# Kernel tuning notes

Measured on AMD Instinct MI355X. Metric: run time of the kernel, lower is better.

## Reference

```python
import jax, jax.numpy as jnp
import numpy as np
import math

B, T, C, E, H = 16, 256, 6, 512, 8


def setup_inputs() -> dict:
    key = jax.random.key(0)
    ks = jax.random.split(key, 5)
    std = 0.02
    return {
        "x": jax.random.normal(ks[0], (B, T, C, E), dtype=jnp.float32),
        "Wq": jax.random.normal(ks[1], (E, E), dtype=jnp.float32) * std,
        "bq": jnp.zeros((E,), dtype=jnp.float32),
        "Wk": jax.random.normal(ks[2], (E, E), dtype=jnp.float32) * std,
        "bk": jnp.zeros((E,), dtype=jnp.float32),
        "Wv": jax.random.normal(ks[3], (E, E), dtype=jnp.float32) * std,
        "bv": jnp.zeros((E,), dtype=jnp.float32),
        "Wp": jax.random.normal(ks[4], (E, E), dtype=jnp.float32) * std,
        "bp": jnp.zeros((E,), dtype=jnp.float32),
    }


def reference(x, Wq, bq, Wk, bk, Wv, bv, Wp, bp):
    b, t, c, e = x.shape
    hd = e // H
    # nn.Linear: y = x @ W^T + b, then view(B,T,C,H,hd).transpose(1,3) -> (B,H,C,T,hd)
    def heads(W, bias):
        y = jnp.einsum('btce,fe->btcf', x, W) + bias
        return y.reshape(b, t, c, H, hd).transpose(0, 3, 2, 1, 4)  # B,H,C,T,hd

    q = heads(Wq, bq)
    k = heads(Wk, bk)
    v = heads(Wv, bv)

    scale = 1.0 / math.sqrt(hd)
    att = jnp.einsum('bhctd,bhcsd->bhcts', q, k) * scale  # B,H,C,T,T
    causal = jnp.tril(jnp.ones((t, t), dtype=bool))
    att = jnp.where(causal, att, -jnp.inf)
    att = jax.nn.softmax(att, axis=-1)

    y = jnp.einsum('bhcts,bhcsd->bhctd', att, v)  # B,H,C,T,hd
    # permute(0,3,1,2,4) -> (B,T,H,C,hd), then view(B,T,C,E) (faithful to torch)
    y = y.transpose(0, 3, 1, 2, 4).reshape(b, t, c, e)
    return jnp.einsum('btce,fe->btcf', y, Wp) + bp
```

## Files before the change

### kernel.cpp

```cpp
#include <hip/hip_runtime.h>


typedef unsigned short u16;
typedef short bf16x8 __attribute__((ext_vector_type(8)));
typedef float f32x4 __attribute__((ext_vector_type(4)));
typedef u16 u16x4 __attribute__((ext_vector_type(4)));

#define MFMA16(a, b, c) __builtin_amdgcn_mfma_f32_16x16x32_bf16((a), (b), (c), 0, 0, 0)

__device__ __forceinline__ u16 f2b(float f) {
  union { float f; unsigned u; } v; v.f = f;
  unsigned r = v.u + 0x7fffu + ((v.u >> 16) & 1u);
  return (u16)(r >> 16);
}
__device__ __forceinline__ void gl_lds16(const void* g, void* l) {
  __builtin_amdgcn_global_load_lds(
      (const __attribute__((address_space(1))) void*)g,
      (__attribute__((address_space(3))) void*)l, 16, 0, 0);
}

__global__ void cvt_all(const float* __restrict__ x, u16* __restrict__ xdst,
                        const float* W0, const float* W1, const float* W2,
                        const float* W3, u16* __restrict__ wdst, int nxb) {
  const int bx = blockIdx.x;
  if (bx < nxb) {
    const size_t idx = ((size_t)bx * 256 + threadIdx.x) * 4;
    f32x4 v = *(const f32x4*)(x + idx);
    u16x4 o; o.x = f2b(v.x); o.y = f2b(v.y); o.z = f2b(v.z); o.w = f2b(v.w);
    *(u16x4*)(xdst + idx) = o;
  } else {
    const int wb = bx - nxb;
    const float* src = (wb < 256) ? W0 : (wb < 512) ? W1
                     : (wb < 768) ? W2 : W3;
    const int idx = ((wb & 255) * 256 + threadIdx.x) * 4;
    f32x4 v = *(const f32x4*)(src + idx);
    u16x4 o; o.x = f2b(v.x); o.y = f2b(v.y); o.z = f2b(v.z); o.w = f2b(v.w);
    *(u16x4*)(wdst + (size_t)(wb >> 8) * 262144 + idx) = o;
  }
}

#define STAGE(k, bi) do { \
  char* Sd_ = Sb + (bi) * 28672; \
  _Pragma("unroll") \
  for (int j_ = 0; j_ < 4; ++j_) \
    if (j_ < 3 || tid < 256) \
      gl_lds16(gsrc[j_] + (k) * 64, Sd_ + fl[j_]); \
} while (0)

__global__ __launch_bounds__(512, 2) void qkv_attn(
    const u16* __restrict__ xbf, const u16* __restrict__ wbf,
    const float* __restrict__ bq, const float* __restrict__ bk,
    const float* __restrict__ bv, u16* __restrict__ y_ws)
{
  const int blk = blockIdx.x;
  const int b   = blk / 48;
  const int h   = (blk / 6) % 8;
  const int c   = blk % 6;

  __shared__ u16 LDS[43008];
  char* Ksb  = (char*)LDS;
  char* Vtsb = (char*)LDS + 16384;
  char* Sb   = (char*)LDS;

  const int tid  = threadIdx.x;
  const int lane = tid & 63;
  const int wv   = tid >> 6;
  const int r    = lane & 15;
  const int qd   = lane >> 4;
  const int tiles[2] = { wv, 15 - wv };
  char* Qw = (char*)LDS + 32768 + wv * 2048;

  const char* gsrc[4]; int fl[4];
  #pragma unroll
  for (int j = 0; j < 4; ++j) {
    const int idx  = j * 512 + tid;
    const int flat = idx * 16;
    const int row  = flat >> 6;
    const int gc   = (((flat >> 4) & 3) - (row >> 1)) & 3;
    fl[j] = flat;
    if (row < 256) {
      gsrc[j] = (const char*)xbf +
                ((size_t)(b * 256 + row) * 6 + c) * 1024 + gc * 16;
    } else {
      const int wr  = row - 256;
      const int tau = (wr >> 6) & 3;
      const int n   = wr & 63;
      gsrc[j] = (const char*)wbf + (size_t)tau * 524288 +
                (size_t)(h * 64 + n) * 1024 + gc * 16;
    }
  }

  int aoff[2], boff[3][4];
  #pragma unroll
  for (int ti = 0; ti < 2; ++ti) {
    const int row = tiles[ti] * 16 + r;
    aoff[ti] = row * 64 + ((qd + (row >> 1)) & 3) * 16;
  }
  #pragma unroll
  for (int tau = 0; tau < 3; ++tau)
    #pragma unroll
    for (int nt = 0; nt < 4; ++nt) {
      const int row = 256 + tau * 64 + nt * 16 + r;
      boff[tau][nt] = row * 64 + ((qd + (row >> 1)) & 3) * 16;
    }

  f32x4 acc[3][2][4] = {};

  STAGE(0, 0);
  STAGE(1, 1);

  #pragma unroll 2
  for (int kt = 0; kt < 16; ++kt) {
    if (kt < 15) { asm volatile("s_waitcnt vmcnt(3)\n\ts_barrier" ::: "memory"); }
    else         { asm volatile("s_waitcnt vmcnt(0)\n\ts_barrier" ::: "memory"); }

    if (kt + 2 < 16) STAGE(kt + 2, (kt + 2) % 3);

    char* Sc = Sb + (kt % 3) * 28672;
    bf16x8 af[2], bfr[3][4];
    #pragma unroll
    for (int ti = 0; ti < 2; ++ti)
      af[ti] = *(const bf16x8*)(Sc + aoff[ti]);
    #pragma unroll
    for (int tau = 0; tau < 3; ++tau)
      #pragma unroll
      for (int nt = 0; nt < 4; ++nt)
        bfr[tau][nt] = *(const bf16x8*)(Sc + boff[tau][nt]);

    #pragma unroll
    for (int tau = 0; tau < 3; ++tau)
      #pragma unroll
      for (int ti = 0; ti < 2; ++ti)
        #pragma unroll
        for (int nt = 0; nt < 4; ++nt)
          acc[tau][ti][nt] = MFMA16(af[ti], bfr[tau][nt], acc[tau][ti][nt]);
  }
  __syncthreads();

  float bqv[4], bkv[4], bvv[4];
  #pragma unroll
  for (int nt = 0; nt < 4; ++nt) {
    const int col = h * 64 + nt * 16 + r;
    bqv[nt] = bq[col]; bkv[nt] = bk[col]; bvv[nt] = bv[col];
  }

  const int lo0 = ( qd      ^ (r & 7)) << 4;
  const int lo1 = ((4 + qd) ^ (r & 7)) << 4;

  f32x4 o_acc[2][4] = {};
  float l_acc[2][4] = {{0.f,0.f,0.f,0.f},{0.f,0.f,0.f,0.f}};

  #pragma unroll
  for (int sc = 0; sc < 2; ++sc) {
    if (sc) __syncthreads();

    {
      const int tl0 = tiles[sc] * 16 + qd * 4 - sc * 128;
      #pragma unroll
      for (int nt = 0; nt < 4; ++nt) {
        u16x4 pv;
        #pragma unroll
        for (int rr = 0; rr < 4; ++rr)
          ((u16*)&pv)[rr] = f2b(acc[2][sc][nt][rr] + bvv[nt]);
        const int vb = (nt * 16 + r) * 256 +
            (((tl0 >> 3) ^ (r & 7)) << 4) + (tl0 & 7) * 2;
        *(u16x4*)(Vtsb + vb) = pv;
      }
      #pragma unroll
      for (int nt = 0; nt < 4; ++nt)
        #pragma unroll
        for (int rr = 0; rr < 4; ++rr) {
          const int tl = tl0 + rr;
          const int kb = tl * 128 +
              (((nt * 2 + (r >> 3)) ^ (tl & 7)) << 4) + (r & 7) * 2;
          *(u16*)(Ksb + kb) = f2b(acc[1][sc][nt][rr] + bkv[nt]);
        }
    }
    __syncthreads();

    #pragma unroll
    for (int ti = 0; ti < 2; ++ti) {
      if (sc == 1 && ti == 0) continue;
      const int mt  = tiles[ti];
      const int i0  = mt * 16;
      const int nch = (mt >> 2) + 1;

      #pragma unroll
      for (int nt = 0; nt < 4; ++nt)
        #pragma unroll
        for (int rr = 0; rr < 4; ++rr) {
          const int prow = qd * 4 + rr;
          const int qb = prow * 128 +
              (((nt * 2 + (r >> 3)) ^ (prow & 7)) << 4) + (r & 7) * 2;
          *(u16*)(Qw + qb) = f2b(acc[0][ti][nt][rr] + bqv[nt]);
        }
      asm volatile("s_waitcnt lgkmcnt(0)" ::: "memory");

      bf16x8 qf[2];
      qf[0] = *(const bf16x8*)(Qw + r * 128 + lo0);
      qf[1] = *(const bf16x8*)(Qw + r * 128 + lo1);
      asm volatile("s_waitcnt lgkmcnt(0)" ::: "memory");

      #pragma unroll
      for (int jcl = 0; jcl < 2; ++jcl) {
        const int jcg = sc * 2 + jcl;
        if (jcg >= nch) continue;
        const int j0l = jcl * 64;
        const int j0g = jcg * 64;

        f32x4 s[4] = {};
        #pragma unroll
        for (int nt = 0; nt < 4; ++nt) {
          const int krow = j0l + nt * 16 + r;
          bf16x8 kf0 = *(const bf16x8*)(Ksb + krow * 128 + lo0);
          s[nt] = MFMA16(qf[0], kf0, s[nt]);
          bf16x8 kf1 = *(const bf16x8*)(Ksb + krow * 128 + lo1);
          s[nt] = MFMA16(qf[1], kf1, s[nt]);
        }

        #pragma unroll
        for (int nt = 0; nt < 4; ++nt)
          #pragma unroll
          for (int rr = 0; rr < 4; ++rr) {
            const int i = i0 + qd * 4 + rr;
            const int j = j0g + nt * 16 + r;
            float p = __builtin_exp2f(fminf(s[nt][rr], 500.f) *
                                      0.1803368801111244f);
            if (j > i) p = 0.f;
            l_acc[ti][rr] += p;
            const int prow = qd * 4 + rr;
            const int pb = prow * 128 +
                (((nt * 2 + (r >> 3)) ^ (prow & 7)) << 4) + (r & 7) * 2;
            *(u16*)(Qw + pb) = f2b(p);
          }
        asm volatile("s_waitcnt lgkmcnt(0)" ::: "memory");

        bf16x8 pf[2];
        pf[0] = *(const bf16x8*)(Qw + r * 128 + lo0);
        pf[1] = *(const bf16x8*)(Qw + r * 128 + lo1);
        #pragma unroll
        for (int ntd = 0; ntd < 4; ++ntd) {
          const int vrow = ntd * 16 + r;
          bf16x8 vf0 = *(const bf16x8*)(Vtsb + vrow * 256 +
              ((((j0l >> 3) + qd) ^ (r & 7)) << 4));
          o_acc[ti][ntd] = MFMA16(pf[0], vf0, o_acc[ti][ntd]);
          bf16x8 vf1 = *(const bf16x8*)(Vtsb + vrow * 256 +
              ((((j0l >> 3) + 4 + qd) ^ (r & 7)) << 4));
          o_acc[ti][ntd] = MFMA16(pf[1], vf1, o_acc[ti][ntd]);
        }
      }
    }
  }

  const size_t obase = ((size_t)b * 256) * 3072 + h * 384 + c * 64;
  #pragma unroll
  for (int ti = 0; ti < 2; ++ti) {
    const int i0 = tiles[ti] * 16;
    float linv[4];
    #pragma unroll
    for (int rr = 0; rr < 4; ++rr) {
      float sum = l_acc[ti][rr];
      sum += __shfl_xor(sum, 1, 16);
      sum += __shfl_xor(sum, 2, 16);
      sum += __shfl_xor(sum, 4, 16);
      sum += __shfl_xor(sum, 8, 16);
      linv[rr] = 1.f / sum;
    }
    #pragma unroll
    for (int ntd = 0; ntd < 4; ++ntd)
      #pragma unroll
      for (int rr = 0; rr < 4; ++rr) {
        const int t = i0 + qd * 4 + rr;
        const int d = ntd * 16 + r;
        y_ws[obase + (size_t)t * 3072 + d] = f2b(o_acc[ti][ntd][rr] * linv[rr]);
      }
  }
}

__global__ __launch_bounds__(256, 3) void gemm_bt(
    const u16* __restrict__ A,
    const u16* W0, const u16* W1, const u16* W2,
    const float* bs0, const float* bs1, const float* bs2,
    u16* O0, u16* O1, u16* O2,
    float* OF,
    int qkv_mode)
{
  const int z = blockIdx.z;
  const u16* W    = (z == 0) ? W0 : (z == 1) ? W1 : W2;
  const float* bs = (z == 0) ? bs0 : (z == 1) ? bs1 : bs2;
  u16* O          = (z == 0) ? O0 : (z == 1) ? O1 : O2;

  const int m0 = blockIdx.x * 128;
  const int n0 = blockIdx.y * 128;

  __shared__ u16 As[128 * 32];
  __shared__ u16 Bs[128 * 32];

  const int tid  = threadIdx.x;
  const int lane = tid & 63;
  const int wv   = tid >> 6;
  const int r    = lane & 15;
  const int qd   = lane >> 4;
  const int wm   = (wv & 1) * 64;
  const int wn   = (wv >> 1) * 64;

  f32x4 acc[4][4] = {};

  for (int k0 = 0; k0 < 512; k0 += 32) {
    __syncthreads();
    #pragma unroll
    for (int it = 0; it < 2; ++it) {
      const int flat = (it * 256 + tid) * 16;
      const int row  = flat >> 6;
      const int swc  = (flat >> 4) & 3;
      const int gc   = (swc - (row >> 1)) & 3;
      gl_lds16((const char*)A + (size_t)(m0 + row) * 1024 + k0 * 2 + gc * 16,
               (char*)As + flat);
      gl_lds16((const char*)W + (size_t)(n0 + row) * 1024 + k0 * 2 + gc * 16,
               (char*)Bs + flat);
    }
    __syncthreads();

    bf16x8 af[4], bf[4];
    #pragma unroll
    for (int mt = 0; mt < 4; ++mt) {
      const int row = wm + mt * 16 + r;
      const int sw  = (qd + (row >> 1)) & 3;
      af[mt] = *(const bf16x8*)((const char*)As + row * 64 + sw * 16);
    }
    #pragma unroll
    for (int nt = 0; nt < 4; ++nt) {
      const int row = wn + nt * 16 + r;
      const int sw  = (qd + (row >> 1)) & 3;
      bf[nt] = *(const bf16x8*)((const char*)Bs + row * 64 + sw * 16);
    }
    #pragma unroll
    for (int mt = 0; mt < 4; ++mt)
      #pragma unroll
      for (int nt = 0; nt < 4; ++nt)
        acc[mt][nt] = MFMA16(af[mt], bf[nt], acc[mt][nt]);
  }

  float bv[4];
  #pragma unroll
  for (int nt = 0; nt < 4; ++nt) bv[nt] = bs[n0 + wn + nt * 16 + r];

  if (qkv_mode) {
    #pragma unroll
    for (int mt = 0; mt < 4; ++mt) {
      #pragma unroll
      for (int rr = 0; rr < 4; ++rr) {
        const int m   = m0 + wm + mt * 16 + qd * 4 + rr;
        const int b   = m / 1536;
        const int rem = m - b * 1536;
        const int t   = rem / 6;
        const int c   = rem - t * 6;
        #pragma unroll
        for (int nt = 0; nt < 4; ++nt) {
          const int f = n0 + wn + nt * 16 + r;
          const int hh = f >> 6;
          const int d = f & 63;
          const size_t addr = ((((size_t)b * 8 + hh) * 6 + c) * 256 + t) * 64 + d;
          O[addr] = f2b(acc[mt][nt][rr] + bv[nt]);
        }
      }
    }
  } else {
    #pragma unroll
    for (int mt = 0; mt < 4; ++mt) {
      #pragma unroll
      for (int rr = 0; rr < 4; ++rr) {
        const int m = m0 + wm + mt * 16 + qd * 4 + rr;
        #pragma unroll
        for (int nt = 0; nt < 4; ++nt) {
          const int f = n0 + wn + nt * 16 + r;
          OF[(size_t)m * 512 + f] = acc[mt][nt][rr] + bv[nt];
        }
      }
    }
  }
}

extern "C" void kernel_launch(void* const* d_in, const int* in_sizes, int n_in,
                              void* d_out, int out_size, void* d_ws, size_t ws_size,
                              hipStream_t stream) {
  const float* x  = (const float*)d_in[0];
  const float* Wq = (const float*)d_in[1];
  const float* bq = (const float*)d_in[2];
  const float* Wk = (const float*)d_in[3];
  const float* bk = (const float*)d_in[4];
  const float* Wv = (const float*)d_in[5];
  const float* bv = (const float*)d_in[6];
  const float* Wp = (const float*)d_in[7];
  const float* bp = (const float*)d_in[8];
  float* out = (float*)d_out;

  const size_t PER_B = 256 * 6 * 512;
  const size_t WSEG  = 4 * 262144;

  int NB = 16;
  while (NB > 1 && (WSEG + (size_t)2 * NB * PER_B) * 2 > ws_size) NB >>= 1;

  u16* wbf = (u16*)d_ws;
  u16* Wpb = wbf + 3 * 262144;

  const size_t slab = (size_t)NB * PER_B;
  u16* xbf  = wbf + WSEG;
  u16* y_ws = xbf + slab;

  const int nslab = 16 / NB;
  for (int s = 0; s < nslab; ++s) {
    const float* x_s  = x   + (size_t)s * NB * PER_B;
    float*      out_s = out + (size_t)s * NB * PER_B;
    const int nxb = NB * 768;
    const int grid = (s == 0) ? nxb + 1024 : nxb;
    cvt_all<<<dim3(grid), 256, 0, stream>>>(x_s, xbf, Wq, Wk, Wv, Wp, wbf, nxb);
    qkv_attn<<<dim3(NB * 48), 512, 0, stream>>>(xbf, wbf, bq, bk, bv, y_ws);
    gemm_bt<<<dim3(NB * 12, 4, 1), 256, 0, stream>>>(
        y_ws, Wpb, Wpb, Wpb, bp, bp, bp, nullptr, nullptr, nullptr, out_s, 0);
  }
}
```

Before: 202.0 us.

## Retile QKV projection per wave and stage full Q in shared memory

Each wave now computes a contiguous 64-row by 32-column block of the Q, K and V projections instead of two scattered 16-row tiles across all 64 head columns. This cuts the LDS fragment loads per k-step from 14 to 10 for the same 24 MFMAs. The full biased Q tile is written once to shared memory after the GEMM, replacing the per-tile Q write, waitcnt and readback inside attention. The P scratch moves to a separate LDS region. K/V writes are now split by wave group per half of the sequence, which changes the LDS layout and bookkeeping.

```diff
diff --git a/kernel.cpp b/kernel.cpp
--- a/kernel.cpp
+++ b/kernel.cpp
@@ -60,6 +60,7 @@
   __shared__ u16 LDS[43008];
   char* Ksb  = (char*)LDS;
   char* Vtsb = (char*)LDS + 16384;
+  char* Qsb  = (char*)LDS + 32768;
   char* Sb   = (char*)LDS;
 
   const int tid  = threadIdx.x;
@@ -67,8 +68,10 @@
   const int wv   = tid >> 6;
   const int r    = lane & 15;
   const int qd   = lane >> 4;
+  const int g    = wv >> 1;
+  const int ch   = wv & 1;
   const int tiles[2] = { wv, 15 - wv };
-  char* Qw = (char*)LDS + 32768 + wv * 2048;
+  char* Pw = (char*)LDS + 65536 + wv * 2048;
 
   const char* gsrc[4]; int fl[4];
   #pragma unroll
@@ -82,29 +85,31 @@
       gsrc[j] = (const char*)xbf +
                 ((size_t)(b * 256 + row) * 6 + c) * 1024 + gc * 16;
     } else {
-      const int wr  = row - 256;
-      const int tau = (wr >> 6) & 3;
-      const int n   = wr & 63;
+      const int sr  = row - 256;
+      const int chw = sr / 96;
+      const int rem = sr - chw * 96;
+      const int tau = rem >> 5;
+      const int nn  = rem & 31;
       gsrc[j] = (const char*)wbf + (size_t)tau * 524288 +
-                (size_t)(h * 64 + n) * 1024 + gc * 16;
-    }
-  }
-
-  int aoff[2], boff[3][4];
-  #pragma unroll
-  for (int ti = 0; ti < 2; ++ti) {
-    const int row = tiles[ti] * 16 + r;
-    aoff[ti] = row * 64 + ((qd + (row >> 1)) & 3) * 16;
+                (size_t)(h * 64 + chw * 32 + nn) * 1024 + gc * 16;
+    }
+  }
+
+  int aoff[4], boff[3][2];
+  #pragma unroll
+  for (int mt = 0; mt < 4; ++mt) {
+    const int row = g * 64 + mt * 16 + r;
+    aoff[mt] = row * 64 + ((qd + (row >> 1)) & 3) * 16;
   }
   #pragma unroll
   for (int tau = 0; tau < 3; ++tau)
     #pragma unroll
-    for (int nt = 0; nt < 4; ++nt) {
-      const int row = 256 + tau * 64 + nt * 16 + r;
+    for (int nt = 0; nt < 2; ++nt) {
+      const int row = 256 + ch * 96 + tau * 32 + nt * 16 + r;
       boff[tau][nt] = row * 64 + ((qd + (row >> 1)) & 3) * 16;
     }
 
-  f32x4 acc[3][2][4] = {};
+  f32x4 acc[3][4][2] = {};
 
   STAGE(0, 0);
   STAGE(1, 1);
@@ -117,36 +122,48 @@
     if (kt + 2 < 16) STAGE(kt + 2, (kt + 2) % 3);
 
     char* Sc = Sb + (kt % 3) * 28672;
-    bf16x8 af[2], bfr[3][4];
-    #pragma unroll
-    for (int ti = 0; ti < 2; ++ti)
-      af[ti] = *(const bf16x8*)(Sc + aoff[ti]);
+    bf16x8 af[4], bfr[3][2];
+    #pragma unroll
+    for (int mt = 0; mt < 4; ++mt)
+      af[mt] = *(const bf16x8*)(Sc + aoff[mt]);
     #pragma unroll
     for (int tau = 0; tau < 3; ++tau)
       #pragma unroll
-      for (int nt = 0; nt < 4; ++nt)
+      for (int nt = 0; nt < 2; ++nt)
         bfr[tau][nt] = *(const bf16x8*)(Sc + boff[tau][nt]);
 
     #pragma unroll
     for (int tau = 0; tau < 3; ++tau)
       #pragma unroll
-      for (int ti = 0; ti < 2; ++ti)
-        #pragma unroll
-        for (int nt = 0; nt < 4; ++nt)
-          acc[tau][ti][nt] = MFMA16(af[ti], bfr[tau][nt], acc[tau][ti][nt]);
+      for (int mt = 0; mt < 4; ++mt)
+        #pragma unroll
+        for (int nt = 0; nt < 2; ++nt)
+          acc[tau][mt][nt] = MFMA16(af[mt], bfr[tau][nt], acc[tau][mt][nt]);
   }
   __syncthreads();
 
-  float bqv[4], bkv[4], bvv[4];
-  #pragma unroll
-  for (int nt = 0; nt < 4; ++nt) {
-    const int col = h * 64 + nt * 16 + r;
+  float bqv[2], bkv[2], bvv[2];
+  #pragma unroll
+  for (int nt = 0; nt < 2; ++nt) {
+    const int col = h * 64 + ch * 32 + nt * 16 + r;
     bqv[nt] = bq[col]; bkv[nt] = bk[col]; bvv[nt] = bv[col];
   }
 
   const int lo0 = ( qd      ^ (r & 7)) << 4;
   const int lo1 = ((4 + qd) ^ (r & 7)) << 4;
 
+  #pragma unroll
+  for (int mt = 0; mt < 4; ++mt)
+    #pragma unroll
+    for (int nt = 0; nt < 2; ++nt)
+      #pragma unroll
+      for (int rr = 0; rr < 4; ++rr) {
+        const int t   = g * 64 + mt * 16 + qd * 4 + rr;
+        const int col = ch * 32 + nt * 16 + r;
+        const int qb  = t * 128 + (((col >> 3) ^ (t & 7)) << 4) + (r & 7) * 2;
+        *(u16*)(Qsb + qb) = f2b(acc[0][mt][nt][rr] + bqv[nt]);
+      }
+
   f32x4 o_acc[2][4] = {};
   float l_acc[2][4] = {{0.f,0.f,0.f,0.f},{0.f,0.f,0.f,0.f}};
 
@@ -154,27 +171,30 @@
   for (int sc = 0; sc < 2; ++sc) {
     if (sc) __syncthreads();
 
-    {
-      const int tl0 = tiles[sc] * 16 + qd * 4 - sc * 128;
-      #pragma unroll
-      for (int nt = 0; nt < 4; ++nt) {
-        u16x4 pv;
-        #pragma unroll
-        for (int rr = 0; rr < 4; ++rr)
-          ((u16*)&pv)[rr] = f2b(acc[2][sc][nt][rr] + bvv[nt]);
-        const int vb = (nt * 16 + r) * 256 +
-            (((tl0 >> 3) ^ (r & 7)) << 4) + (tl0 & 7) * 2;
-        *(u16x4*)(Vtsb + vb) = pv;
-      }
-      #pragma unroll
-      for (int nt = 0; nt < 4; ++nt)
-        #pragma unroll
-        for (int rr = 0; rr < 4; ++rr) {
-          const int tl = tl0 + rr;
-          const int kb = tl * 128 +
-              (((nt * 2 + (r >> 3)) ^ (tl & 7)) << 4) + (r & 7) * 2;
-          *(u16*)(Ksb + kb) = f2b(acc[1][sc][nt][rr] + bkv[nt]);
+    if ((g >> 1) == sc) {
+      #pragma unroll
+      for (int mt = 0; mt < 4; ++mt) {
+        const int tl0 = g * 64 + mt * 16 + qd * 4 - sc * 128;
+        #pragma unroll
+        for (int nt = 0; nt < 2; ++nt) {
+          u16x4 pv;
+          #pragma unroll
+          for (int rr = 0; rr < 4; ++rr)
+            ((u16*)&pv)[rr] = f2b(acc[2][mt][nt][rr] + bvv[nt]);
+          const int d  = ch * 32 + nt * 16 + r;
+          const int vb = d * 256 + (((tl0 >> 3) ^ (r & 7)) << 4) + (tl0 & 7) * 2;
+          *(u16x4*)(Vtsb + vb) = pv;
         }
+        #pragma unroll
+        for (int nt = 0; nt < 2; ++nt)
+          #pragma unroll
+          for (int rr = 0; rr < 4; ++rr) {
+            const int tl  = tl0 + rr;
+            const int col = ch * 32 + nt * 16 + r;
+            const int kb  = tl * 128 + (((col >> 3) ^ (tl & 7)) << 4) + (r & 7) * 2;
+            *(u16*)(Ksb + kb) = f2b(acc[1][mt][nt][rr] + bkv[nt]);
+          }
+      }
     }
     __syncthreads();
 
@@ -185,21 +205,9 @@
       const int i0  = mt * 16;
       const int nch = (mt >> 2) + 1;
 
-      #pragma unroll
-      for (int nt = 0; nt < 4; ++nt)
-        #pragma unroll
-        for (int rr = 0; rr < 4; ++rr) {
-          const int prow = qd * 4 + rr;
-          const int qb = prow * 128 +
-              (((nt * 2 + (r >> 3)) ^ (prow & 7)) << 4) + (r & 7) * 2;
-          *(u16*)(Qw + qb) = f2b(acc[0][ti][nt][rr] + bqv[nt]);
-        }
-      asm volatile("s_waitcnt lgkmcnt(0)" ::: "memory");
-
       bf16x8 qf[2];
-      qf[0] = *(const bf16x8*)(Qw + r * 128 + lo0);
-      qf[1] = *(const bf16x8*)(Qw + r * 128 + lo1);
-      asm volatile("s_waitcnt lgkmcnt(0)" ::: "memory");
+      qf[0] = *(const bf16x8*)(Qsb + (i0 + r) * 128 + lo0);
+      qf[1] = *(const bf16x8*)(Qsb + (i0 + r) * 128 + lo1);
 
       #pragma unroll
       for (int jcl = 0; jcl < 2; ++jcl) {
@@ -231,13 +239,13 @@
             const int prow = qd * 4 + rr;
             const int pb = prow * 128 +
                 (((nt * 2 + (r >> 3)) ^ (prow & 7)) << 4) + (r & 7) * 2;
-            *(u16*)(Qw + pb) = f2b(p);
+            *(u16*)(Pw + pb) = f2b(p);
           }
         asm volatile("s_waitcnt lgkmcnt(0)" ::: "memory");
 
         bf16x8 pf[2];
-        pf[0] = *(const bf16x8*)(Qw + r * 128 + lo0);
-        pf[1] = *(const bf16x8*)(Qw + r * 128 + lo1);
+        pf[0] = *(const bf16x8*)(Pw + r * 128 + lo0);
+        pf[1] = *(const bf16x8*)(Pw + r * 128 + lo1);
         #pragma unroll
         for (int ntd = 0; ntd < 4; ++ntd) {
           const int vrow = ntd * 16 + r;
```

Measured after the change: 202.7 us. Within noise of the previous version (+0.4%).
